# Kernel tuning notes

Hardware: AMD Instinct MI355X
Metric: run time of the kernel (lower is better)

Reference implementation:

```python
import jax, jax.numpy as jnp
import numpy as np

N = 100_000   # nodes
E = 1_600_000 # edges
D = 128       # hidden/input dim
OUT = 32      # output dim
G = 512       # graphs in batch
L = 3         # conv layers


def setup_inputs() -> dict:
    key = jax.random.key(0)
    ks = jax.random.split(key, 12)
    s = 1.0 / np.sqrt(D)
    inp = {
        "x": jax.random.normal(ks[0], (N, D), jnp.float32),
        "edge_index": jax.random.randint(ks[1], (2, E), 0, N, dtype=jnp.int32),
        "batch": jnp.sort(jax.random.randint(ks[2], (N,), 0, G, dtype=jnp.int32)),
        "enc_W1": jax.random.normal(ks[3], (D, D), jnp.float32) * s,
        "enc_b1": jnp.zeros((D,), jnp.float32),
        "enc_W2": jax.random.normal(ks[4], (D, D), jnp.float32) * s,
        "enc_b2": jnp.zeros((D,), jnp.float32),
        "gcn_W": jax.random.normal(ks[5], (L, D, D), jnp.float32) * s,
        "gcn_b": jnp.zeros((L, D), jnp.float32),
        "dec_W1": jax.random.normal(ks[6], (D, D), jnp.float32) * s,
        "dec_b1": jnp.zeros((D,), jnp.float32),
        "dec_W2": jax.random.normal(ks[7], (D, OUT), jnp.float32) * s,
        "dec_b2": jnp.zeros((OUT,), jnp.float32),
        "num_graphs": G,
    }
    return inp


def reference(x, edge_index, batch, enc_W1, enc_b1, enc_W2, enc_b2,
              gcn_W, gcn_b, dec_W1, dec_b1, dec_W2, dec_b2, num_graphs):
    n = x.shape[0]
    src, dst = edge_index[0], edge_index[1]

    # ---- encoder MLP (Linear -> ReLU -> Linear -> ReLU) ----
    h = jax.nn.relu(x @ enc_W1 + enc_b1)
    h = jax.nn.relu(h @ enc_W2 + enc_b2)

    # ---- GCN normalization: D^{-1/2} (A + I) D^{-1/2}, degrees incl. self-loops ----
    deg = jax.ops.segment_sum(jnp.ones_like(src, dtype=h.dtype), dst, num_segments=n) + 1.0
    inv_sqrt = jax.lax.rsqrt(deg)           # [N]
    edge_coef = inv_sqrt[src] * inv_sqrt[dst]  # [E]
    self_coef = inv_sqrt * inv_sqrt            # [N]

    # ---- GCN conv layers ----
    for l in range(gcn_W.shape[0]):
        hw = h @ gcn_W[l]                                       # [N, D]
        msgs = hw[src] * edge_coef[:, None]                     # [E, D] gather
        agg = jax.ops.segment_sum(msgs, dst, num_segments=n)    # [N, D] scatter-add
        agg = agg + hw * self_coef[:, None]                     # self loops
        h = jax.nn.relu(agg + gcn_b[l])

    # ---- global add pool over graphs ----
    pooled = jax.ops.segment_sum(h, batch, num_segments=num_graphs)  # [G, D]

    # ---- decoder MLP ----
    out = jax.nn.relu(pooled @ dec_W1 + dec_b1)
    return out @ dec_W2 + dec_b2
```

## Files before the change

kernel.cpp:

```cpp
#include <hip/hip_runtime.h>

#define NNODES 100000
#define NEDGES 1600000
#define DIM    128
#define OUTD   32
#define NGRAPH 512

#define NBUCK2  256
#define BSHIFT  9
#define CAP     12288
#define EPB2    8192
#define SBLOCKS ((NEDGES + EPB2 - 1) / EPB2)
#define PREPBLK 160
#define NBUILD  ((NNODES + 511) / 512)
#define EBLK64  ((NNODES + 63) / 64)
#define AGGBLK  ((NNODES + 31) / 32)
#define NZERO   (NBUCK2 + NGRAPH * DIM + NNODES)
#define ZBLOCKS ((NZERO + 511) / 512)

using bf16x8 = __attribute__((ext_vector_type(8))) short;
using f32x4  = __attribute__((ext_vector_type(4))) float;
using f32x2  = __attribute__((ext_vector_type(2))) float;

__device__ __forceinline__ short f2bf(float f) {
    unsigned u = __float_as_uint(f);
    unsigned r = (u + 0x7fff + ((u >> 16) & 1)) >> 16;
    return (short)r;
}
__device__ __forceinline__ float bf2f(short s) {
    return __uint_as_float(((unsigned)(unsigned short)s) << 16);
}

__device__ __forceinline__ uint2 bf8_to_fp8(bf16x8 t) {
    float f0 = bf2f(t[0]), f1 = bf2f(t[1]), f2 = bf2f(t[2]), f3 = bf2f(t[3]);
    float f4 = bf2f(t[4]), f5 = bf2f(t[5]), f6 = bf2f(t[6]), f7 = bf2f(t[7]);
    uint2 o;
    o.x = __builtin_amdgcn_cvt_pk_fp8_f32(f0, f1, 0, false);
    o.x = __builtin_amdgcn_cvt_pk_fp8_f32(f2, f3, o.x, true);
    o.y = __builtin_amdgcn_cvt_pk_fp8_f32(f4, f5, 0, false);
    o.y = __builtin_amdgcn_cvt_pk_fp8_f32(f6, f7, o.y, true);
    return o;
}

__global__ __launch_bounds__(512) void k_zero(int* __restrict__ gz)
{
    int idx = blockIdx.x * 512 + threadIdx.x;
    if (idx < NZERO) gz[idx] = 0;
}

__global__ __launch_bounds__(512) void k_scatter_prep(
    const int* __restrict__ src, const int* __restrict__ dst,
    int* __restrict__ gcur, unsigned* __restrict__ tmp,
    int* __restrict__ deg,
    const float* __restrict__ eW1, const float* __restrict__ eW2,
    const float* __restrict__ gW, short* __restrict__ WT)
{
    const int tid = threadIdx.x;

    if (blockIdx.x >= SBLOCKS) {
        int idx = (blockIdx.x - SBLOCKS) * 512 + tid;
        int mat = idx >> 14, rem = idx & 16383;
        int k = rem >> 7, n = rem & 127;
        const float* sp = (mat == 0) ? eW1 : (mat == 1) ? eW2
                                           : (gW + (size_t)(mat - 2) * 16384);
        WT[(size_t)mat * 16384 + n * DIM + k] = f2bf(sp[k * DIM + n]);
        return;
    }

    __shared__ unsigned short rnk[EPB2];
    __shared__ int h[NBUCK2];
    __shared__ int gbase[NBUCK2];
    const int base = blockIdx.x * EPB2;
    if (tid < NBUCK2) h[tid] = 0;
    __syncthreads();
    #pragma unroll
    for (int it = 0; it < EPB2 / 512; ++it) {
        int e = base + it * 512 + tid;
        if (e < NEDGES) {
            int d = dst[e];
            rnk[it * 512 + tid] = (unsigned short)atomicAdd(&h[d >> BSHIFT], 1);
            atomicAdd(&deg[d], 1);
        }
    }
    __syncthreads();
    if (tid < NBUCK2 && h[tid] > 0)
        gbase[tid] = tid * CAP + atomicAdd(&gcur[tid], h[tid]);
    __syncthreads();
    #pragma unroll
    for (int it = 0; it < EPB2 / 512; ++it) {
        int e = base + it * 512 + tid;
        if (e < NEDGES) {
            int d = dst[e], sv = src[e];
            int b = d >> BSHIFT;
            int pos = gbase[b] + rnk[it * 512 + tid];
            if (pos < (b + 1) * CAP)
                tmp[pos] = (unsigned)sv | ((unsigned)(d & 511) << 17);
        }
    }
}

__global__ __launch_bounds__(512, 6) void k_build_enc(
    const unsigned* __restrict__ tmp, const int* __restrict__ gcur,
    int* __restrict__ row_off, int* __restrict__ cntA,
    float* __restrict__ inv, int* __restrict__ col,
    const int* __restrict__ deg,
    const float* __restrict__ x, const short* __restrict__ WT,
    const float* __restrict__ b1, const float* __restrict__ b2,
    unsigned char* __restrict__ g8, int M)
{
    __shared__ short As[64 * 128];
    __shared__ short Bs[128 * 128];

    const int tid = threadIdx.x;

    if (blockIdx.x < NBUILD) {
        int* hist = (int*)As;
        int* sc   = hist + 512;
        int* lcur = sc + 512;
        const int b     = blockIdx.x;
        const int tbase = b * CAP;
        const int cnt_b = min(gcur[b], CAP);
        hist[tid] = 0;
        __syncthreads();
        for (int i = tid; i < cnt_b; i += 512)
            atomicAdd(&hist[(tmp[tbase + i] >> 17) & 511], 1);
        __syncthreads();
        const int hv = hist[tid];
        sc[tid] = hv;
        __syncthreads();
        for (int off = 1; off < 512; off <<= 1) {
            int t = (tid >= off) ? sc[tid - off] : 0;
            __syncthreads();
            sc[tid] += t;
            __syncthreads();
        }
        const int start = tbase + sc[tid] - hv;
        lcur[tid] = start;
        const int node = b * 512 + tid;
        if (node < NNODES) {
            row_off[node] = start;
            cntA[node]    = hv;
            inv[node]     = rsqrtf((float)hv + 1.0f);
        }
        __syncthreads();
        for (int i = tid; i < cnt_b; i += 512) {
            unsigned t = tmp[tbase + i];
            int pos = atomicAdd(&lcur[(t >> 17) & 511], 1);
            col[pos] = (int)((t & 0x1FFFFu) << 7);
        }
        return;
    }

    const int m0 = (blockIdx.x - NBUILD) * 64;

    #pragma unroll
    for (int i = 0; i < 2; ++i) {
        int u = tid + i * 512;
        int row = u >> 4, c = u & 15;
        int gr = min(m0 + row, M - 1);
        const float4* sp = (const float4*)(x + (size_t)gr * DIM + (c << 3));
        float4 f0 = sp[0], f1 = sp[1];
        short t8[8] = { f2bf(f0.x), f2bf(f0.y), f2bf(f0.z), f2bf(f0.w),
                        f2bf(f1.x), f2bf(f1.y), f2bf(f1.z), f2bf(f1.w) };
        *(bf16x8*)&As[row * 128 + ((c ^ (row & 15)) << 3)] = *(bf16x8*)t8;
    }

    const int wave = tid >> 6, lane = tid & 63;
    const int ml = lane & 15, quad = lane >> 4;
    const int rw = wave >> 1;
    const int cw = wave & 1;

    #pragma unroll
    for (int mat = 0; mat < 3; ++mat) {
        if (mat > 0) __syncthreads();
        #pragma unroll
        for (int i = 0; i < 4; ++i) {
            int u = tid + i * 512;
            int n = u >> 4, c = u & 15;
            *(bf16x8*)&Bs[n * 128 + ((c ^ (n & 15)) << 3)] =
                *(const bf16x8*)(WT + (size_t)mat * 16384 + n * DIM + (c << 3));
        }
        __syncthreads();

        f32x4 acc[4] = {};
        const int arow = rw * 16 + ml;
        #pragma unroll
        for (int kk = 0; kk < 4; ++kk) {
            const int c = kk * 4 + quad;
            bf16x8 a = *(bf16x8*)&As[arow * 128 + ((c ^ (arow & 15)) << 3)];
            #pragma unroll
            for (int ni = 0; ni < 4; ++ni) {
                const int brow = (cw * 4 + ni) * 16 + ml;
                bf16x8 b = *(bf16x8*)&Bs[brow * 128 + ((c ^ (brow & 15)) << 3)];
                acc[ni] = __builtin_amdgcn_mfma_f32_16x16x32_bf16(a, b, acc[ni], 0, 0, 0);
            }
        }
        __syncthreads();

        #pragma unroll
        for (int ni = 0; ni < 4; ++ni) {
            const int colc = cw * 64 + ni * 16 + ml;
            const int cc = colc >> 3, w = colc & 7;
            #pragma unroll
            for (int r = 0; r < 4; ++r) {
                const int rowl = rw * 16 + quad * 4 + r;
                float v = acc[ni][r];
                if (mat == 0)      v = fmaxf(v + b1[colc], 0.f);
                else if (mat == 1) v = fmaxf(v + b2[colc], 0.f);
                else
                    v *= rsqrtf((float)deg[min(m0 + rowl, M - 1)] + 1.0f);
                As[rowl * 128 + (((cc ^ (rowl & 15)) << 3) | w)] = f2bf(v);
            }
        }
    }
    __syncthreads();

    #pragma unroll
    for (int i = 0; i < 2; ++i) {
        int u = tid + i * 512;
        int row = u >> 4, c = u & 15;
        int gr = m0 + row;
        if (gr < M) {
            bf16x8 t = *(bf16x8*)&As[row * 128 + ((c ^ (row & 15)) << 3)];
            *(uint2*)(g8 + (size_t)gr * DIM + (c << 3)) = bf8_to_fp8(t);
        }
    }
}

#define GATHER_PIPELINE()                                                      \
    const int rs = row_off[node];                                              \
    const int re = rs + cntA[node];                                            \
    int j = rs;                                                                \
    {                                                                          \
        uint2 b0, b1_, b2_, b3_, b4_, b5_, b6_, b7_;                           \
        const bool hav = (j + 7 < re);                                         \
        if (hav) {                                                             \
            b0 = GLD(col[j]);     b1_ = GLD(col[j + 1]);                       \
            b2_ = GLD(col[j + 2]); b3_ = GLD(col[j + 3]);                      \
            b4_ = GLD(col[j + 4]); b5_ = GLD(col[j + 5]);                      \
            b6_ = GLD(col[j + 6]); b7_ = GLD(col[j + 7]);                      \
            j += 8;                                                            \
        }                                                                      \
        for (; j + 7 < re; j += 8) {                                           \
            uint2 n0 = GLD(col[j]);     uint2 n1 = GLD(col[j + 1]);            \
            uint2 n2 = GLD(col[j + 2]); uint2 n3 = GLD(col[j + 3]);            \
            uint2 n4 = GLD(col[j + 4]); uint2 n5 = GLD(col[j + 5]);            \
            uint2 n6 = GLD(col[j + 6]); uint2 n7 = GLD(col[j + 7]);            \
            ACC8(b0) ACC8(b1_) ACC8(b2_) ACC8(b3_)                             \
            ACC8(b4_) ACC8(b5_) ACC8(b6_) ACC8(b7_)                            \
            b0 = n0; b1_ = n1; b2_ = n2; b3_ = n3;                             \
            b4_ = n4; b5_ = n5; b6_ = n6; b7_ = n7;                            \
        }                                                                      \
        if (hav) {                                                             \
            ACC8(b0) ACC8(b1_) ACC8(b2_) ACC8(b3_)                             \
            ACC8(b4_) ACC8(b5_) ACC8(b6_) ACC8(b7_)                            \
        }                                                                      \
    }                                                                          \
    for (; j + 3 < re; j += 4) {                                               \
        uint2 v0 = GLD(col[j]);     uint2 v1 = GLD(col[j + 1]);                \
        uint2 v2 = GLD(col[j + 2]); uint2 v3 = GLD(col[j + 3]);                \
        ACC8(v0) ACC8(v1) ACC8(v2) ACC8(v3)                                    \
    }                                                                          \
    for (; j < re; ++j) {                                                      \
        uint2 v = GLD(col[j]);                                                 \
        ACC8(v)                                                                \
    }

__global__ __launch_bounds__(512, 8) void k_agg_gemm(
    const unsigned char* __restrict__ g8v, const int* __restrict__ row_off,
    const int* __restrict__ cntA, const int* __restrict__ col,
    const float* __restrict__ inv, const float* __restrict__ bias,
    const short* __restrict__ WT, unsigned char* __restrict__ g8o)
{
    __shared__ short As[32 * 128];
    __shared__ short Bs[128 * 128];

    const int tid = threadIdx.x;

    #pragma unroll
    for (int i = 0; i < 4; ++i) {
        int u = tid + i * 512;
        int n = u >> 4, c = u & 15;
        *(bf16x8*)&Bs[n * 128 + ((c ^ (n & 15)) << 3)] =
            *(const bf16x8*)(WT + n * DIM + (c << 3));
    }

    const int wave = tid >> 6, lane = tid & 63;
    const int q    = lane >> 4;
    const int sl   = lane & 15;
    const int sl8  = sl << 3;
    const int nl   = wave * 4 + q;
    const int m0   = blockIdx.x * 32;
    const int node = m0 + nl;

    f32x2 a01, a23, a45, a67;
    {
        uint2 us = *(const uint2*)(g8v + (size_t)node * 128 + sl8);
        a01 = __builtin_amdgcn_cvt_pk_f32_fp8(us.x, false);
        a23 = __builtin_amdgcn_cvt_pk_f32_fp8(us.x, true);
        a45 = __builtin_amdgcn_cvt_pk_f32_fp8(us.y, false);
        a67 = __builtin_amdgcn_cvt_pk_f32_fp8(us.y, true);
    }

    #define ACC8(v) \
        a01 += __builtin_amdgcn_cvt_pk_f32_fp8(v.x, false); \
        a23 += __builtin_amdgcn_cvt_pk_f32_fp8(v.x, true);  \
        a45 += __builtin_amdgcn_cvt_pk_f32_fp8(v.y, false); \
        a67 += __builtin_amdgcn_cvt_pk_f32_fp8(v.y, true);
    #define GLD(c) (*(const uint2*)(g8v + (size_t)(unsigned)((c) + sl8)))

    GATHER_PIPELINE()

    #undef ACC8
    #undef GLD

    const float scv = inv[node];
    const float4 bb0 = ((const float4*)bias)[sl * 2];
    const float4 bb1 = ((const float4*)bias)[sl * 2 + 1];
    short o[8];
    o[0] = f2bf(fmaxf(fmaf(a01[0], scv, bb0.x), 0.f));
    o[1] = f2bf(fmaxf(fmaf(a01[1], scv, bb0.y), 0.f));
    o[2] = f2bf(fmaxf(fmaf(a23[0], scv, bb0.z), 0.f));
    o[3] = f2bf(fmaxf(fmaf(a23[1], scv, bb0.w), 0.f));
    o[4] = f2bf(fmaxf(fmaf(a45[0], scv, bb1.x), 0.f));
    o[5] = f2bf(fmaxf(fmaf(a45[1], scv, bb1.y), 0.f));
    o[6] = f2bf(fmaxf(fmaf(a67[0], scv, bb1.z), 0.f));
    o[7] = f2bf(fmaxf(fmaf(a67[1], scv, bb1.w), 0.f));
    *(bf16x8*)&As[nl * 128 + ((sl ^ (nl & 15)) << 3)] = *(bf16x8*)o;
    __syncthreads();

    const int mh = wave >> 2;
    const int nq = wave & 3;
    f32x4 acc[2] = {};
    #pragma unroll
    for (int kk = 0; kk < 4; ++kk) {
        const int c = kk * 4 + q;
        bf16x8 a = *(bf16x8*)&As[(mh * 16 + sl) * 128 + ((c ^ sl) << 3)];
        #pragma unroll
        for (int ni = 0; ni < 2; ++ni) {
            bf16x8 b = *(bf16x8*)&Bs[((nq * 2 + ni) * 16 + sl) * 128 + ((c ^ sl) << 3)];
            acc[ni] = __builtin_amdgcn_mfma_f32_16x16x32_bf16(a, b, acc[ni], 0, 0, 0);
        }
    }
    __syncthreads();

    #pragma unroll
    for (int ni = 0; ni < 2; ++ni) {
        const int colc = (nq * 2 + ni) * 16 + sl;
        const int cc   = colc >> 3, cw = colc & 7;
        #pragma unroll
        for (int r = 0; r < 4; ++r) {
            const int rowl = mh * 16 + q * 4 + r;
            As[rowl * 128 + (((cc ^ (rowl & 15)) << 3) | cw)] =
                f2bf(acc[ni][r] * inv[m0 + rowl]);
        }
    }
    __syncthreads();

    {
        int row = tid >> 4, c = tid & 15;
        bf16x8 t = *(bf16x8*)&As[row * 128 + ((c ^ (row & 15)) << 3)];
        *(uint2*)(g8o + (size_t)(m0 + row) * DIM + (c << 3)) = bf8_to_fp8(t);
    }
}

__global__ __launch_bounds__(512) void k_agg_pool(
    const unsigned char* __restrict__ g8v, const int* __restrict__ row_off,
    const int* __restrict__ cntA, const int* __restrict__ col,
    const float* __restrict__ inv, const float* __restrict__ bias,
    const int* __restrict__ batch, float* __restrict__ pooled)
{
    __shared__ float Hs[32][132];
    __shared__ int sbatch[32];

    const int tid = threadIdx.x;
    const int wave = tid >> 6, lane = tid & 63;
    const int q    = lane >> 4;
    const int sl   = lane & 15;
    const int sl8  = sl << 3;
    const int nl   = wave * 4 + q;
    const int m0   = blockIdx.x * 32;
    const int node = m0 + nl;

    if (tid < 32) sbatch[tid] = batch[m0 + tid];

    f32x2 a01, a23, a45, a67;
    {
        uint2 us = *(const uint2*)(g8v + (size_t)node * 128 + sl8);
        a01 = __builtin_amdgcn_cvt_pk_f32_fp8(us.x, false);
        a23 = __builtin_amdgcn_cvt_pk_f32_fp8(us.x, true);
        a45 = __builtin_amdgcn_cvt_pk_f32_fp8(us.y, false);
        a67 = __builtin_amdgcn_cvt_pk_f32_fp8(us.y, true);
    }

    #define ACC8(v) \
        a01 += __builtin_amdgcn_cvt_pk_f32_fp8(v.x, false); \
        a23 += __builtin_amdgcn_cvt_pk_f32_fp8(v.x, true);  \
        a45 += __builtin_amdgcn_cvt_pk_f32_fp8(v.y, false); \
        a67 += __builtin_amdgcn_cvt_pk_f32_fp8(v.y, true);
    #define GLD(c) (*(const uint2*)(g8v + (size_t)(unsigned)((c) + sl8)))

    GATHER_PIPELINE()

    #undef ACC8
    #undef GLD

    const float scv = inv[node];
    const float4 bb0 = ((const float4*)bias)[sl * 2];
    const float4 bb1 = ((const float4*)bias)[sl * 2 + 1];
    float4 h0, h1;
    h0.x = fmaxf(fmaf(a01[0], scv, bb0.x), 0.f);
    h0.y = fmaxf(fmaf(a01[1], scv, bb0.y), 0.f);
    h0.z = fmaxf(fmaf(a23[0], scv, bb0.z), 0.f);
    h0.w = fmaxf(fmaf(a23[1], scv, bb0.w), 0.f);
    h1.x = fmaxf(fmaf(a45[0], scv, bb1.x), 0.f);
    h1.y = fmaxf(fmaf(a45[1], scv, bb1.y), 0.f);
    h1.z = fmaxf(fmaf(a67[0], scv, bb1.z), 0.f);
    h1.w = fmaxf(fmaf(a67[1], scv, bb1.w), 0.f);
    *(float4*)&Hs[nl][sl * 8]     = h0;
    *(float4*)&Hs[nl][sl * 8 + 4] = h1;
    __syncthreads();

    const int d   = tid & 127;
    const int grp = tid >> 7;
    float acc = 0.f;
    int cg = -1;
    #pragma unroll
    for (int i = 0; i < 8; ++i) {
        const int nn = grp * 8 + i;
        const int g  = sbatch[nn];
        if (g != cg) {
            if (cg >= 0) atomicAdd(pooled + (size_t)cg * DIM + d, acc);
            cg = g; acc = 0.f;
        }
        acc += Hs[nn][d];
    }
    atomicAdd(pooled + (size_t)cg * DIM + d, acc);
}

__global__ __launch_bounds__(512) void k_dec(
    const float* __restrict__ pooled, const float* __restrict__ W1,
    const float* __restrict__ b1, const float* __restrict__ W2,
    const float* __restrict__ b2, float* __restrict__ out)
{
    __shared__ float pbuf[8][128];
    __shared__ float tbuf[8][128];
    const int wave = threadIdx.x >> 6, lane = threadIdx.x & 63;
    const int g = blockIdx.x * 8 + wave;

    float2 pv = *(const float2*)(pooled + (size_t)g * DIM + lane * 2);
    pbuf[wave][lane * 2]     = pv.x;
    pbuf[wave][lane * 2 + 1] = pv.y;
    __syncthreads();

    float t0 = 0.f, t1 = 0.f;
    #pragma unroll 8
    for (int k = 0; k < DIM; ++k) {
        float pk = pbuf[wave][k];
        float2 w = *(const float2*)(W1 + (size_t)k * DIM + lane * 2);
        t0 = fmaf(pk, w.x, t0);
        t1 = fmaf(pk, w.y, t1);
    }
    tbuf[wave][lane * 2]     = fmaxf(t0 + b1[lane * 2],     0.f);
    tbuf[wave][lane * 2 + 1] = fmaxf(t1 + b1[lane * 2 + 1], 0.f);
    __syncthreads();

    const int c = lane & 31, hh = lane >> 5;
    float part = 0.f;
    #pragma unroll 8
    for (int kk = 0; kk < 64; ++kk) {
        int k = hh * 64 + kk;
        part = fmaf(tbuf[wave][k], W2[(size_t)k * OUTD + c], part);
    }
    float other = __shfl_xor(part, 32, 64);
    if (hh == 0)
        out[(size_t)g * OUTD + c] = part + other + b2[c];
}

extern "C" void kernel_launch(void* const* d_in, const int* in_sizes, int n_in,
                              void* d_out, int out_size, void* d_ws, size_t ws_size,
                              hipStream_t stream)
{
    const float* x      = (const float*)d_in[0];
    const int*   ei     = (const int*)d_in[1];
    const int*   batch  = (const int*)d_in[2];
    const float* enc_W1 = (const float*)d_in[3];
    const float* enc_b1 = (const float*)d_in[4];
    const float* enc_W2 = (const float*)d_in[5];
    const float* enc_b2 = (const float*)d_in[6];
    const float* gcn_W  = (const float*)d_in[7];
    const float* gcn_b  = (const float*)d_in[8];
    const float* dec_W1 = (const float*)d_in[9];
    const float* dec_b1 = (const float*)d_in[10];
    const float* dec_W2 = (const float*)d_in[11];
    const float* dec_b2 = (const float*)d_in[12];
    float* out = (float*)d_out;

    const int* src = ei;
    const int* dst = ei + NEDGES;

    char* p = (char*)d_ws;
    auto alloc = [&](size_t bytes) -> void* {
        void* r = (void*)p;
        p += (bytes + 255) & ~(size_t)255;
        return r;
    };
    int*           gcur   = (int*)          alloc((size_t)NBUCK2 * sizeof(int));
    float*         pooled = (float*)        alloc((size_t)NGRAPH * DIM * sizeof(float));
    int*           deg    = (int*)          alloc((size_t)NNODES * sizeof(int));
    unsigned char* g8a    = (unsigned char*)alloc((size_t)NNODES * DIM);
    unsigned char* g8b    = (unsigned char*)alloc((size_t)NNODES * DIM);
    float*         inv    = (float*)        alloc((size_t)NNODES * sizeof(float));
    int*           row_off= (int*)          alloc((size_t)NNODES * sizeof(int));
    int*           cntA   = (int*)          alloc((size_t)NNODES * sizeof(int));
    int*           col    = (int*)          alloc((size_t)NBUCK2 * CAP * sizeof(int));
    unsigned*      tmp    = (unsigned*)     alloc((size_t)NBUCK2 * CAP * sizeof(unsigned));
    short*         WT     = (short*)        alloc((size_t)5 * DIM * DIM * sizeof(short));

    k_zero<<<ZBLOCKS, 512, 0, stream>>>(gcur);

    k_scatter_prep<<<SBLOCKS + PREPBLK, 512, 0, stream>>>(
        src, dst, gcur, tmp, deg, enc_W1, enc_W2, gcn_W, WT);

    k_build_enc<<<NBUILD + EBLK64, 512, 0, stream>>>(
        tmp, gcur, row_off, cntA, inv, col, deg,
        x, WT, enc_b1, enc_b2, g8a, NNODES);

    k_agg_gemm<<<AGGBLK, 512, 0, stream>>>(g8a, row_off, cntA, col, inv,
                                           gcn_b,       WT + 3 * 16384, g8b);
    k_agg_gemm<<<AGGBLK, 512, 0, stream>>>(g8b, row_off, cntA, col, inv,
                                           gcn_b + 128, WT + 4 * 16384, g8a);
    k_agg_pool<<<AGGBLK, 512, 0, stream>>>(g8a, row_off, cntA, col, inv,
                                           gcn_b + 256, batch, pooled);

    k_dec <<<NGRAPH / 8, 512, 0, stream>>>(pooled, dec_W1, dec_b1,
                                           dec_W2, dec_b2, out);
}
```

Measured before the change: 340.1 us.

## Drop global degree atomics; split first GCN GEMM into separate kernel using inv

Removes the per-edge global atomicAdd on a degree array during scatter prep, and instead uses the inv array computed by the CSR build. The encoder kernel now stops after two layers and writes bf16 hidden state to a new buffer. A new kernel then applies the first GCN weight, scales by inv and writes fp8. This trades 1.6M global atomics for an extra launch and a bf16 round trip through memory.

```diff
diff --git a/kernel.cpp b/kernel.cpp
--- a/kernel.cpp
+++ b/kernel.cpp
@@ -15,7 +15,7 @@
 #define NBUILD  ((NNODES + 511) / 512)
 #define EBLK64  ((NNODES + 63) / 64)
 #define AGGBLK  ((NNODES + 31) / 32)
-#define NZERO   (NBUCK2 + NGRAPH * DIM + NNODES)
+#define NZERO   (NBUCK2 + NGRAPH * DIM)
 #define ZBLOCKS ((NZERO + 511) / 512)
 
 using bf16x8 = __attribute__((ext_vector_type(8))) short;
@@ -51,7 +51,6 @@
 __global__ __launch_bounds__(512) void k_scatter_prep(
     const int* __restrict__ src, const int* __restrict__ dst,
     int* __restrict__ gcur, unsigned* __restrict__ tmp,
-    int* __restrict__ deg,
     const float* __restrict__ eW1, const float* __restrict__ eW2,
     const float* __restrict__ gW, short* __restrict__ WT)
 {
@@ -77,9 +76,8 @@
     for (int it = 0; it < EPB2 / 512; ++it) {
         int e = base + it * 512 + tid;
         if (e < NEDGES) {
-            int d = dst[e];
-            rnk[it * 512 + tid] = (unsigned short)atomicAdd(&h[d >> BSHIFT], 1);
-            atomicAdd(&deg[d], 1);
+            int b = dst[e] >> BSHIFT;
+            rnk[it * 512 + tid] = (unsigned short)atomicAdd(&h[b], 1);
         }
     }
     __syncthreads();
@@ -99,14 +97,13 @@
     }
 }
 
-__global__ __launch_bounds__(512, 6) void k_build_enc(
+__global__ __launch_bounds__(512, 6) void k_build_enc01(
     const unsigned* __restrict__ tmp, const int* __restrict__ gcur,
     int* __restrict__ row_off, int* __restrict__ cntA,
     float* __restrict__ inv, int* __restrict__ col,
-    const int* __restrict__ deg,
     const float* __restrict__ x, const short* __restrict__ WT,
     const float* __restrict__ b1, const float* __restrict__ b2,
-    unsigned char* __restrict__ g8, int M)
+    short* __restrict__ hbuf, int M)
 {
     __shared__ short As[64 * 128];
     __shared__ short Bs[128 * 128];
@@ -171,7 +168,7 @@
     const int cw = wave & 1;
 
     #pragma unroll
-    for (int mat = 0; mat < 3; ++mat) {
+    for (int mat = 0; mat < 2; ++mat) {
         if (mat > 0) __syncthreads();
         #pragma unroll
         for (int i = 0; i < 4; ++i) {
@@ -205,10 +202,7 @@
             for (int r = 0; r < 4; ++r) {
                 const int rowl = rw * 16 + quad * 4 + r;
                 float v = acc[ni][r];
-                if (mat == 0)      v = fmaxf(v + b1[colc], 0.f);
-                else if (mat == 1) v = fmaxf(v + b2[colc], 0.f);
-                else
-                    v *= rsqrtf((float)deg[min(m0 + rowl, M - 1)] + 1.0f);
+                v = fmaxf(v + ((mat == 0) ? b1[colc] : b2[colc]), 0.f);
                 As[rowl * 128 + (((cc ^ (rowl & 15)) << 3) | w)] = f2bf(v);
             }
         }
@@ -221,9 +215,70 @@
         int row = u >> 4, c = u & 15;
         int gr = m0 + row;
         if (gr < M) {
-            bf16x8 t = *(bf16x8*)&As[row * 128 + ((c ^ (row & 15)) << 3)];
-            *(uint2*)(g8 + (size_t)gr * DIM + (c << 3)) = bf8_to_fp8(t);
-        }
+            *(bf16x8*)(hbuf + (size_t)gr * DIM + (c << 3)) =
+                *(bf16x8*)&As[row * 128 + ((c ^ (row & 15)) << 3)];
+        }
+    }
+}
+
+__global__ __launch_bounds__(512, 8) void k_enc2(
+    const short* __restrict__ hbuf, const short* __restrict__ WT,
+    const float* __restrict__ inv, unsigned char* __restrict__ g8)
+{
+    __shared__ short As[32 * 128];
+    __shared__ short Bs[128 * 128];
+
+    const int tid = threadIdx.x;
+    const int m0  = blockIdx.x * 32;
+
+    #pragma unroll
+    for (int i = 0; i < 4; ++i) {
+        int u = tid + i * 512;
+        int n = u >> 4, c = u & 15;
+        *(bf16x8*)&Bs[n * 128 + ((c ^ (n & 15)) << 3)] =
+            *(const bf16x8*)(WT + n * DIM + (c << 3));
+    }
+    {
+        int row = tid >> 4, c = tid & 15;
+        *(bf16x8*)&As[row * 128 + ((c ^ (row & 15)) << 3)] =
+            *(const bf16x8*)(hbuf + (size_t)(m0 + row) * DIM + (c << 3));
+    }
+    __syncthreads();
+
+    const int wave = tid >> 6, lane = tid & 63;
+    const int q  = lane >> 4, sl = lane & 15;
+    const int mh = wave >> 2;
+    const int nq = wave & 3;
+    f32x4 acc[2] = {};
+    #pragma unroll
+    for (int kk = 0; kk < 4; ++kk) {
+        const int c = kk * 4 + q;
+        bf16x8 a = *(bf16x8*)&As[(mh * 16 + sl) * 128 + ((c ^ sl) << 3)];
+        #pragma unroll
+        for (int ni = 0; ni < 2; ++ni) {
+            bf16x8 b = *(bf16x8*)&Bs[((nq * 2 + ni) * 16 + sl) * 128 + ((c ^ sl) << 3)];
+            acc[ni] = __builtin_amdgcn_mfma_f32_16x16x32_bf16(a, b, acc[ni], 0, 0, 0);
+        }
+    }
+    __syncthreads();
+
+    #pragma unroll
+    for (int ni = 0; ni < 2; ++ni) {
+        const int colc = (nq * 2 + ni) * 16 + sl;
+        const int cc = colc >> 3, cw = colc & 7;
+        #pragma unroll
+        for (int r = 0; r < 4; ++r) {
+            const int rowl = mh * 16 + q * 4 + r;
+            As[rowl * 128 + (((cc ^ (rowl & 15)) << 3) | cw)] =
+                f2bf(acc[ni][r] * inv[m0 + rowl]);
+        }
+    }
+    __syncthreads();
+
+    {
+        int row = tid >> 4, c = tid & 15;
+        bf16x8 t = *(bf16x8*)&As[row * 128 + ((c ^ (row & 15)) << 3)];
+        *(uint2*)(g8 + (size_t)(m0 + row) * DIM + (c << 3)) = bf8_to_fp8(t);
     }
 }
 
@@ -507,9 +562,9 @@
     };
     int*           gcur   = (int*)          alloc((size_t)NBUCK2 * sizeof(int));
     float*         pooled = (float*)        alloc((size_t)NGRAPH * DIM * sizeof(float));
-    int*           deg    = (int*)          alloc((size_t)NNODES * sizeof(int));
     unsigned char* g8a    = (unsigned char*)alloc((size_t)NNODES * DIM);
     unsigned char* g8b    = (unsigned char*)alloc((size_t)NNODES * DIM);
+    short*         hbuf   = (short*)        alloc((size_t)NNODES * DIM * sizeof(short));
     float*         inv    = (float*)        alloc((size_t)NNODES * sizeof(float));
     int*           row_off= (int*)          alloc((size_t)NNODES * sizeof(int));
     int*           cntA   = (int*)          alloc((size_t)NNODES * sizeof(int));
@@ -520,11 +575,13 @@
     k_zero<<<ZBLOCKS, 512, 0, stream>>>(gcur);
 
     k_scatter_prep<<<SBLOCKS + PREPBLK, 512, 0, stream>>>(
-        src, dst, gcur, tmp, deg, enc_W1, enc_W2, gcn_W, WT);
-
-    k_build_enc<<<NBUILD + EBLK64, 512, 0, stream>>>(
-        tmp, gcur, row_off, cntA, inv, col, deg,
-        x, WT, enc_b1, enc_b2, g8a, NNODES);
+        src, dst, gcur, tmp, enc_W1, enc_W2, gcn_W, WT);
+
+    k_build_enc01<<<NBUILD + EBLK64, 512, 0, stream>>>(
+        tmp, gcur, row_off, cntA, inv, col,
+        x, WT, enc_b1, enc_b2, hbuf, NNODES);
+
+    k_enc2<<<AGGBLK, 512, 0, stream>>>(hbuf, WT + 2 * 16384, inv, g8a);
 
     k_agg_gemm<<<AGGBLK, 512, 0, stream>>>(g8a, row_off, cntA, col, inv,
                                            gcn_b,       WT + 3 * 16384, g8b);
```

Result: faster. 293.5 us, median of 2 (-13.7%).
